# Performance work log

Measured on AMD Instinct MI355X. Metric: run time of the kernel, lower is better.

Reference implementation:

```python
import jax, jax.numpy as jnp
import numpy as np

D_MODEL = 1024
NUM_HEAD = 16
BATCH = 2
SEQ = 2048
NEG_INF = -1e9  # matches masked_fill value in the original


def setup_inputs() -> dict:
    key = jax.random.key(0)
    k1, k2, k3, k4, k5 = jax.random.split(key, 5)
    scale = 1.0 / np.sqrt(D_MODEL)
    return {
        "x": jax.random.normal(k1, (BATCH, SEQ, D_MODEL), dtype=jnp.float32),
        "q_weight": jax.random.normal(k2, (D_MODEL, D_MODEL), dtype=jnp.float32) * scale,
        "k_weight": jax.random.normal(k3, (D_MODEL, D_MODEL), dtype=jnp.float32) * scale,
        "v_weight": jax.random.normal(k4, (D_MODEL, D_MODEL), dtype=jnp.float32) * scale,
        "o_weight": jax.random.normal(k5, (D_MODEL, D_MODEL), dtype=jnp.float32) * scale,
    }


def reference(x, q_weight, k_weight, v_weight, o_weight):
    b, s, d = x.shape
    h = NUM_HEAD
    dh = d // h
    # projections: weight layout is (d_out, d_in)
    q = jnp.einsum('bsd,ed->bse', x, q_weight).reshape(b, s, h, dh).transpose(0, 2, 1, 3)
    k = jnp.einsum('bsd,ed->bse', x, k_weight).reshape(b, s, h, dh).transpose(0, 2, 1, 3)
    v = jnp.einsum('bsd,ed->bse', x, v_weight).reshape(b, s, h, dh).transpose(0, 2, 1, 3)
    scores = jnp.einsum('bhqd,bhkd->bhqk', q, k) / jnp.sqrt(jnp.asarray(dh, x.dtype))
    causal = jnp.triu(jnp.ones((s, s), dtype=bool), k=1)  # True above diagonal -> masked
    scores = jnp.where(causal, jnp.asarray(NEG_INF, x.dtype), scores)
    attn = jax.nn.softmax(scores, axis=-1)
    out = jnp.einsum('bhqk,bhkd->bhqd', attn, v)          # [b,h,s,dh]
    out = out.transpose(0, 2, 1, 3).reshape(b, s, d)       # merge heads
    return jnp.einsum('bse,de->bsd', out, o_weight)
```

## Files before the change

kernel.cpp:

```cpp
#include <hip/hip_runtime.h>

typedef short bhalf8 __attribute__((ext_vector_type(8)));
typedef float floatx4 __attribute__((ext_vector_type(4)));

#define D_MODEL 1024
#define SEQ     2048
#define BATCH   2
#define NHEAD   16
#define DH      64

#define GLDS(g, l) __builtin_amdgcn_global_load_lds( \
    (const __attribute__((address_space(1))) void*)(g), \
    (__attribute__((address_space(3))) void*)(l), 16, 0, 0)

static __device__ __forceinline__ short f2bf(float f) {
    unsigned u = __builtin_bit_cast(unsigned, f);
    u = (u + 0x7fffu + ((u >> 16) & 1u)) >> 16;
    return (short)u;
}
static __device__ __forceinline__ unsigned pack2(float a, float b) {
    return (unsigned)(unsigned short)f2bf(a) | ((unsigned)(unsigned short)f2bf(b) << 16);
}
static __device__ __forceinline__ unsigned cvt_pk_bf16(float lo, float hi) {
    unsigned r;
    asm("v_cvt_pk_bf16_f32 %0, %1, %2" : "=v"(r) : "v"(lo), "v"(hi));
    return r;
}

__global__ __launch_bounds__(256) void cast_all(const float* __restrict__ x,
                                                const float* __restrict__ wq,
                                                const float* __restrict__ wk,
                                                const float* __restrict__ wv,
                                                const float* __restrict__ wo,
                                                short* __restrict__ xb,
                                                short* __restrict__ wall) {
    const int bid = blockIdx.x;
    const float* s;
    short* d;
    int i;
    if (bid < 2048) {
        s = x; d = xb;
        i = (bid * 256 + threadIdx.x) * 8;
    } else {
        const int wb = bid - 2048;
        const int which = wb >> 9;
        s = (which == 0) ? wq : (which == 1) ? wk : (which == 2) ? wv : wo;
        d = wall + (size_t)which * (D_MODEL * D_MODEL);
        i = ((wb & 511) * 256 + threadIdx.x) * 8;
    }
    float4 a = *(const float4*)(s + i);
    float4 b = *(const float4*)(s + i + 4);
    uint4 u = {pack2(a.x, a.y), pack2(a.z, a.w), pack2(b.x, b.y), pack2(b.z, b.w)};
    *(uint4*)(d + i) = u;
}

#define MFMA_BF16 __builtin_amdgcn_mfma_f32_16x16x32_bf16

#define QISSUE(kt, s) do {                                                    \
    char* ab_ = pool + (s) * 16384 + (w * 32) * 64;                           \
    char* bb_ = pool + 49152 + (s) * 16384 + (w * 32) * 64;                   \
    GLDS(Ag + (size_t)(kt) * 32, ab_);                                        \
    GLDS(Ag + (size_t)(kt) * 32 + 16 * 1024, ab_ + 1024);                     \
    GLDS(Wg + (size_t)(kt) * 32, bb_);                                        \
    GLDS(Wg + (size_t)(kt) * 32 + 16 * 1024, bb_ + 1024);                     \
} while (0)

#define QCOMP(s) do {                                                         \
    const short(*As_)[32] = (const short(*)[32])(pool + (s) * 16384);         \
    const short(*Bs_)[32] = (const short(*)[32])(pool + 49152 + (s) * 16384); \
    bhalf8 af_[8], bf_[4];                                                    \
    _Pragma("unroll")                                                         \
    for (int m_ = 0; m_ < 8; ++m_)                                            \
        af_[m_] = *(const bhalf8*)&As_[wr * 128 + m_ * 16 + l16][quad * 8];   \
    _Pragma("unroll")                                                         \
    for (int n_ = 0; n_ < 4; ++n_)                                            \
        bf_[n_] = *(const bhalf8*)&Bs_[wc * 64 + n_ * 16 + l16][quad * 8];    \
    __builtin_amdgcn_s_setprio(1);                                            \
    _Pragma("unroll")                                                         \
    for (int m_ = 0; m_ < 8; ++m_)                                            \
        _Pragma("unroll")                                                     \
        for (int n_ = 0; n_ < 4; ++n_)                                        \
            acc[m_][n_] = MFMA_BF16(af_[m_], bf_[n_], acc[m_][n_], 0, 0, 0);  \
    __builtin_amdgcn_s_setprio(0);                                            \
} while (0)

__global__ __launch_bounds__(512) void gemm_qkv2(const short* __restrict__ A,
                                                 const short* __restrict__ W,
                                                 short* __restrict__ Qo,
                                                 short* __restrict__ Ko,
                                                 short* __restrict__ Vt) {
    __shared__ __align__(16) char pool[98304];
    const int t    = threadIdx.x;
    const int w    = t >> 6, lane = t & 63, quad = lane >> 4, l16 = lane & 15;
    const int wr   = w >> 2, wc = w & 3;
    const int bm   = blockIdx.x * 256;
    const int by   = (int)blockIdx.y;
    const int bn   = by * 256;

    const short* Ag = A + (size_t)(bm + w * 32 + (lane >> 2)) * 1024 + (lane & 3) * 8;
    const short* Wg = W + (size_t)(bn + w * 32 + (lane >> 2)) * 1024 + (lane & 3) * 8;

    floatx4 acc[8][4];
#pragma unroll
    for (int m = 0; m < 8; ++m)
#pragma unroll
        for (int n = 0; n < 4; ++n) {
            floatx4 z = {0.f, 0.f, 0.f, 0.f};
            acc[m][n] = z;
        }

    QISSUE(0, 0);
    QISSUE(1, 1);
    int sc_ = 0, sn_ = 2;
#pragma unroll 1
    for (int kt = 0; kt < 30; ++kt) {
        asm volatile("s_waitcnt vmcnt(4)" ::: "memory");
        __builtin_amdgcn_s_barrier();
        QISSUE(kt + 2, sn_);
        QCOMP(sc_);
        sc_ = (sc_ == 2) ? 0 : sc_ + 1;
        sn_ = (sn_ == 2) ? 0 : sn_ + 1;
    }
    asm volatile("s_waitcnt vmcnt(4)" ::: "memory");
    __builtin_amdgcn_s_barrier();
    QCOMP(sc_);
    sc_ = (sc_ == 2) ? 0 : sc_ + 1;
    asm volatile("s_waitcnt vmcnt(0)" ::: "memory");
    __builtin_amdgcn_s_barrier();
    QCOMP(sc_);

    __syncthreads();
    short (*Ct)[268] = (short(*)[268])pool;
    if (by < 8) {
        short* outp = (by < 4) ? Qo : Ko;
        const int colbase = (by < 4) ? bn : bn - 1024;
        for (int hh = 0; hh < 2; ++hh) {
            if (wr == hh) {
#pragma unroll
                for (int m = 0; m < 8; ++m)
#pragma unroll
                    for (int n = 0; n < 4; ++n)
#pragma unroll
                        for (int g = 0; g < 4; ++g)
                            Ct[m * 16 + quad * 4 + g][wc * 64 + n * 16 + l16] =
                                f2bf(acc[m][n][g]);
            }
            __syncthreads();
            {
                const int r = t >> 2, c0 = (t & 3) * 64;
#pragma unroll
                for (int p = 0; p < 8; ++p)
                    *(uint4*)(outp + (size_t)(bm + hh * 128 + r) * 1024 +
                              colbase + c0 + p * 8) =
                        *(const uint4*)&Ct[r][c0 + p * 8];
            }
            __syncthreads();
        }
    } else {
        const int nbase = bn - 2048;
        for (int hh = 0; hh < 2; ++hh) {
            if ((wc >> 1) == hh) {
#pragma unroll
                for (int m = 0; m < 8; ++m)
#pragma unroll
                    for (int n = 0; n < 4; ++n)
#pragma unroll
                        for (int g = 0; g < 4; ++g)
                            Ct[wc * 64 + n * 16 + l16 - hh * 128]
                              [wr * 128 + m * 16 + quad * 4 + g] =
                                f2bf(acc[m][n][g]);
            }
            __syncthreads();
            {
                const int r = t >> 2, c0 = (t & 3) * 64;
#pragma unroll
                for (int p = 0; p < 8; ++p)
                    *(uint4*)(Vt + (size_t)(nbase + hh * 128 + r) * 4096 +
                              bm + c0 + p * 8) =
                        *(const uint4*)&Ct[r][c0 + p * 8];
            }
            __syncthreads();
        }
    }
}

__global__ __launch_bounds__(256) void gemm_o(const short* __restrict__ A,
                                              const short* __restrict__ W,
                                              float* __restrict__ C) {
    __shared__ __align__(16) char pool[34816];
    short (*As)[64] = (short(*)[64])pool;
    short (*Bs)[64] = (short(*)[64])(pool + 16384);
    const int t    = threadIdx.x;
    const int wave = t >> 6, lane = t & 63, quad = lane >> 4, l16 = lane & 15;
    const int bm = blockIdx.x * 128, bn = blockIdx.y * 64;
    const int qm = (wave >> 1) * 64, qn = (wave & 1) * 32;

    const int lrow = lane >> 3, lcol = (lane & 7) * 8;
    const short* Ag = A + (size_t)(bm + wave * 32 + lrow) * 1024 + lcol;
    const short* Wg = W + (size_t)(bn + wave * 16 + lrow) * 1024 + lcol;
    short* Al = &As[wave * 32][0];
    short* Bl = &Bs[wave * 16][0];

    floatx4 acc[4][2];
#pragma unroll
    for (int i = 0; i < 4; ++i)
#pragma unroll
        for (int j = 0; j < 2; ++j) {
            floatx4 z = {0.f, 0.f, 0.f, 0.f};
            acc[i][j] = z;
        }

    for (int k0 = 0; k0 < 1024; k0 += 64) {
        __syncthreads();
#pragma unroll
        for (int j = 0; j < 4; ++j)
            GLDS(Ag + k0 + (size_t)j * 8 * 1024, Al + j * 8 * 64);
#pragma unroll
        for (int j = 0; j < 2; ++j)
            GLDS(Wg + k0 + (size_t)j * 8 * 1024, Bl + j * 8 * 64);
        __syncthreads();
#pragma unroll
        for (int kk = 0; kk < 64; kk += 32) {
            bhalf8 af[4], bfr[2];
#pragma unroll
            for (int im = 0; im < 4; ++im)
                af[im] = *(const bhalf8*)&As[qm + im * 16 + l16][kk + quad * 8];
#pragma unroll
            for (int jn = 0; jn < 2; ++jn)
                bfr[jn] = *(const bhalf8*)&Bs[qn + jn * 16 + l16][kk + quad * 8];
#pragma unroll
            for (int im = 0; im < 4; ++im)
#pragma unroll
                for (int jn = 0; jn < 2; ++jn)
                    acc[im][jn] = __builtin_amdgcn_mfma_f32_16x16x32_bf16(
                        af[im], bfr[jn], acc[im][jn], 0, 0, 0);
        }
    }

    __syncthreads();
    float (*Ctf)[68] = (float(*)[68])pool;
#pragma unroll
    for (int im = 0; im < 4; ++im)
#pragma unroll
        for (int jn = 0; jn < 2; ++jn)
#pragma unroll
            for (int g = 0; g < 4; ++g)
                Ctf[qm + im * 16 + quad * 4 + g][qn + jn * 16 + l16] = acc[im][jn][g];
    __syncthreads();
#pragma unroll
    for (int pass = 0; pass < 8; ++pass) {
        const int r = (t >> 4) + pass * 16;
        const int c = (t & 15) * 4;
        float4 u = *(const float4*)&Ctf[r][c];
        *(float4*)(C + (size_t)(bm + r) * 1024 + bn + c) = u;
    }
}


#define STAGE_LOAD(kregv, vregv, kk) do {                                     \
    kregv = *(const uint4*)(Kbase + (size_t)((kk) + sr) * 1024 + sc);         \
    vregv = *(const uint4*)(Vbase + (size_t)sr * 4096 + (kk) + sc);           \
    } while (0)

#define STAGE_WRITE(bufv, kregv, vregv) do {                                  \
    *(uint4*)&Ks[bufv][sr][sc] = kregv;                                       \
    *(uint4*)&Vs[bufv][sr][sc] = vregv;                                       \
    } while (0)

#define CHUNK13(bufv, k0v, qwv) do {                                          \
    bhalf8 kf_[4][2];                                                         \
    _Pragma("unroll")                                                         \
    for (int jn_ = 0; jn_ < 4; ++jn_) {                                       \
        kf_[jn_][0] = *(const bhalf8*)&Ks[bufv][jn_ * 16 + l16][quad * 8];    \
        kf_[jn_][1] = *(const bhalf8*)&Ks[bufv][jn_ * 16 + l16][32 + quad * 8]; \
    }                                                                         \
    floatx4 s_[4];                                                            \
    _Pragma("unroll")                                                         \
    for (int jn_ = 0; jn_ < 4; ++jn_) {                                       \
        floatx4 z_ = {0.f, 0.f, 0.f, 0.f};                                    \
        z_ = MFMA_BF16(qf0, kf_[jn_][0], z_, 0, 0, 0);                        \
        z_ = MFMA_BF16(qf1, kf_[jn_][1], z_, 0, 0, 0);                        \
        s_[jn_] = z_;                                                         \
    }                                                                         \
    bhalf8 vf_[4][2];              \
    _Pragma("unroll")                                                         \
    for (int nd_ = 0; nd_ < 4; ++nd_) {                                       \
        vf_[nd_][0] = *(const bhalf8*)&Vs[bufv][nd_ * 16 + l16][quad * 8];    \
        vf_[nd_][1] = *(const bhalf8*)&Vs[bufv][nd_ * 16 + l16][32 + quad * 8]; \
    }                                                                         \
    const bool partial_ = ((k0v) + 64 > (qwv));                               \
    _Pragma("unroll")                                                         \
    for (int g_ = 0; g_ < 4; ++g_) {                                          \
        const int rr_ = quad * 4 + g_;                                        \
        const int qrow_ = (qwv) + rr_;                                        \
        float e0_ = exp2f(s_[0][g_] * KS - CB);                               \
        float e1_ = exp2f(s_[1][g_] * KS - CB);                               \
        float e2_ = exp2f(s_[2][g_] * KS - CB);                               \
        float e3_ = exp2f(s_[3][g_] * KS - CB);                               \
        if (partial_) {                                                       \
            if ((k0v) + l16 > qrow_)      e0_ = 0.f;                          \
            if ((k0v) + 16 + l16 > qrow_) e1_ = 0.f;                          \
            if ((k0v) + 32 + l16 > qrow_) e2_ = 0.f;                          \
            if ((k0v) + 48 + l16 > qrow_) e3_ = 0.f;                          \
        }                                                                     \
        lsum[g_] += (e0_ + e1_) + (e2_ + e3_);                                \
        unsigned r01_ = cvt_pk_bf16(e0_, e1_);                                \
        unsigned r23_ = cvt_pk_bf16(e2_, e3_);                                \
        Ps[wave][rr_][l16]      = (short)r01_;                                \
        Ps[wave][rr_][16 + l16] = (short)(r01_ >> 16);                        \
        Ps[wave][rr_][32 + l16] = (short)r23_;                                \
        Ps[wave][rr_][48 + l16] = (short)(r23_ >> 16);                        \
    }                                                                         \
          \
    bhalf8 ap0_ = *(const bhalf8*)&Ps[wave][l16][quad * 8];                   \
    bhalf8 ap1_ = *(const bhalf8*)&Ps[wave][l16][32 + quad * 8];              \
    _Pragma("unroll")                                                         \
    for (int nd_ = 0; nd_ < 4; ++nd_) {                                       \
        o[nd_] = MFMA_BF16(ap0_, vf_[nd_][0], o[nd_], 0, 0, 0);               \
        o[nd_] = MFMA_BF16(ap1_, vf_[nd_][1], o[nd_], 0, 0, 0);               \
    }                                                                         \
} while (0)

#define SWEEP(qtv, ncv) do {                                                  \
    const int qw_ = (qtv) * 128 + wave * 16;                                  \
    const short* qr_ = Qbase + (size_t)(qw_ + l16) * 1024;                    \
    bhalf8 qf0 = *(const bhalf8*)(qr_ + quad * 8);                            \
    bhalf8 qf1 = *(const bhalf8*)(qr_ + 32 + quad * 8);                       \
    _Pragma("unroll")                                                         \
    for (int g_ = 0; g_ < 4; ++g_) lsum[g_] = 0.f;                            \
    _Pragma("unroll")                                                         \
    for (int nd_ = 0; nd_ < 4; ++nd_) {                                       \
        floatx4 z_ = {0.f, 0.f, 0.f, 0.f};                                    \
        o[nd_] = z_;                                                          \
    }                                                                         \
    uint4 kreg_, vreg_;                                                       \
    STAGE_LOAD(kreg_, vreg_, 0);                                              \
    STAGE_WRITE(0, kreg_, vreg_);                                             \
    if ((ncv) > 1) STAGE_LOAD(kreg_, vreg_, 64);                              \
    __syncthreads();                                                          \
    _Pragma("unroll 1")                                                       \
    for (int i_ = 0; i_ < (ncv); ++i_) {                                      \
        const int buf_ = i_ & 1;                                              \
        if (i_ + 1 < (ncv)) STAGE_WRITE(buf_ ^ 1, kreg_, vreg_);              \
        if (i_ + 2 < (ncv)) STAGE_LOAD(kreg_, vreg_, (i_ + 2) * 64);          \
        CHUNK13(buf_, i_ * 64, qw_);                                          \
        __syncthreads();                                                      \
    }                                                                         \
    _Pragma("unroll")                                                         \
    for (int g_ = 0; g_ < 4; ++g_) {                                          \
        float r_ = lsum[g_];                                                  \
        r_ += __shfl_xor(r_, 1, 64);                                          \
        r_ += __shfl_xor(r_, 2, 64);                                          \
        r_ += __shfl_xor(r_, 4, 64);                                          \
        r_ += __shfl_xor(r_, 8, 64);                                          \
        const float iv_ = 1.0f / r_;                                          \
        const int qrow_ = qw_ + quad * 4 + g_;                                \
        _Pragma("unroll")                                                     \
        for (int nd_ = 0; nd_ < 4; ++nd_)                                     \
            Y[(size_t)(b * SEQ + qrow_) * 1024 + h * 64 + nd_ * 16 + l16] =   \
                f2bf(o[nd_][g_] * iv_);                                       \
    }                                                                         \
} while (0)

__global__ __launch_bounds__(512) void attn_v14(const short* __restrict__ Qo,
                                                const short* __restrict__ Ko,
                                                const short* __restrict__ Vt,
                                                short* __restrict__ Y) {
    __shared__ __align__(16) short Ks[2][64][72];
    __shared__ __align__(16) short Vs[2][64][72];
    __shared__ __align__(16) short Ps[8][16][72];

    const int t    = threadIdx.x;
    const int wave = t >> 6, lane = t & 63, quad = lane >> 4, l16 = lane & 15;
    const int bid  = (int)blockIdx.x;
    const int bh   = bid & 31;
    const int p    = (bid & 255) >> 5;
    const int qt   = (bid < 256) ? (15 - p) : p;
    const int b = bh >> 4, h = bh & 15;

    const short* Qbase = Qo + (size_t)b * SEQ * 1024 + h * 64;
    const short* Kbase = Ko + (size_t)b * SEQ * 1024 + h * 64;
    const short* Vbase = Vt + (size_t)h * 64 * 4096 + (size_t)b * SEQ;

    const int sr = t >> 3;
    const int sc = (t & 7) * 8;

    const float KS = 0.125f * 1.44269504f;
    const float CB = 12.0f * 1.44269504f;

    float lsum[4];
    floatx4 o[4];

    SWEEP(qt, (qt + 1) * 2);
}

extern "C" void kernel_launch(void* const* d_in, const int* in_sizes, int n_in,
                              void* d_out, int out_size, void* d_ws, size_t ws_size,
                              hipStream_t stream) {
    const float* x  = (const float*)d_in[0];
    const float* wq = (const float*)d_in[1];
    const float* wk = (const float*)d_in[2];
    const float* wv = (const float*)d_in[3];
    const float* wo = (const float*)d_in[4];

    short* xb   = (short*)d_ws;
    short* Qo   = xb + (size_t)4096 * 1024;
    short* Ko   = Qo + (size_t)4096 * 1024;
    short* Vt   = Ko + (size_t)4096 * 1024;
    short* wall = Vt + (size_t)1024 * 4096;
    short* wob  = wall + (size_t)3 * 1024 * 1024;

    cast_all<<<dim3(4096), 256, 0, stream>>>(x, wq, wk, wv, wo, xb, wall);
    gemm_qkv2<<<dim3(16, 12), 512, 0, stream>>>(xb, wall, Qo, Ko, Vt);
    attn_v14<<<dim3(512), 512, 0, stream>>>(Qo, Ko, Vt, xb);
    gemm_o<<<dim3(32, 16), 256, 0, stream>>>(xb, wob, (float*)d_out);
}
```

Measured before the change: 190.1 us.

## Split attention key range across two wave teams with per-wave 32-row Q tiles

Restructures the attention kernel so each block's 8 waves form two teams of 4. Each team processes half of the causal key range in 32-key chunks. Each wave now owns 32 query rows instead of 16, so K fragments are reused across two row tiles. The teams' partial O and row-sum results are combined through shared memory before normalisation. The aim is to shorten the serial key loop per block and raise MFMA reuse, at the cost of an extra LDS combine step, more registers, and wasted work when a team's chunks are fully masked. The block-to-query-tile ordering is also reversed.

```diff
diff --git a/kernel.cpp b/kernel.cpp
--- a/kernel.cpp
+++ b/kernel.cpp
@@ -257,141 +257,174 @@
 }
 
 
-#define STAGE_LOAD(kregv, vregv, kk) do {                                     \
-    kregv = *(const uint4*)(Kbase + (size_t)((kk) + sr) * 1024 + sc);         \
-    vregv = *(const uint4*)(Vbase + (size_t)sr * 4096 + (kk) + sc);           \
+#define STAGE_LOAD15(kk) do {                                                 \
+    kreg = *(const uint4*)(Kbase + (size_t)((kk) + skr) * 1024 + skc);        \
+    vreg = *(const uint4*)(Vbase + (size_t)svr * 4096 + (kk) + svc);          \
     } while (0)
 
-#define STAGE_WRITE(bufv, kregv, vregv) do {                                  \
-    *(uint4*)&Ks[bufv][sr][sc] = kregv;                                       \
-    *(uint4*)&Vs[bufv][sr][sc] = vregv;                                       \
+#define STAGE_WRITE15(bufv) do {                                              \
+    *(uint4*)&Ks[team][bufv][skr][skc] = kreg;                                \
+    *(uint4*)&Vs[team][bufv][svr][svc] = vreg;                                \
     } while (0)
 
-#define CHUNK13(bufv, k0v, qwv) do {                                          \
-    bhalf8 kf_[4][2];                                                         \
-    _Pragma("unroll")                                                         \
-    for (int jn_ = 0; jn_ < 4; ++jn_) {                                       \
-        kf_[jn_][0] = *(const bhalf8*)&Ks[bufv][jn_ * 16 + l16][quad * 8];    \
-        kf_[jn_][1] = *(const bhalf8*)&Ks[bufv][jn_ * 16 + l16][32 + quad * 8]; \
+#define CHUNK15(bufv, k0v) do {                                               \
+    bhalf8 kf_[2][2];                                                         \
+    _Pragma("unroll")                                                         \
+    for (int jn_ = 0; jn_ < 2; ++jn_) {                                       \
+        kf_[jn_][0] = *(const bhalf8*)&Ks[team][bufv][jn_ * 16 + l16][quad * 8]; \
+        kf_[jn_][1] = *(const bhalf8*)&Ks[team][bufv][jn_ * 16 + l16][32 + quad * 8]; \
     }                                                                         \
-    floatx4 s_[4];                                                            \
-    _Pragma("unroll")                                                         \
-    for (int jn_ = 0; jn_ < 4; ++jn_) {                                       \
-        floatx4 z_ = {0.f, 0.f, 0.f, 0.f};                                    \
-        z_ = MFMA_BF16(qf0, kf_[jn_][0], z_, 0, 0, 0);                        \
-        z_ = MFMA_BF16(qf1, kf_[jn_][1], z_, 0, 0, 0);                        \
-        s_[jn_] = z_;                                                         \
-    }                                                                         \
-    bhalf8 vf_[4][2];              \
-    _Pragma("unroll")                                                         \
-    for (int nd_ = 0; nd_ < 4; ++nd_) {                                       \
-        vf_[nd_][0] = *(const bhalf8*)&Vs[bufv][nd_ * 16 + l16][quad * 8];    \
-        vf_[nd_][1] = *(const bhalf8*)&Vs[bufv][nd_ * 16 + l16][32 + quad * 8]; \
-    }                                                                         \
-    const bool partial_ = ((k0v) + 64 > (qwv));                               \
-    _Pragma("unroll")                                                         \
-    for (int g_ = 0; g_ < 4; ++g_) {                                          \
-        const int rr_ = quad * 4 + g_;                                        \
-        const int qrow_ = (qwv) + rr_;                                        \
-        float e0_ = exp2f(s_[0][g_] * KS - CB);                               \
-        float e1_ = exp2f(s_[1][g_] * KS - CB);                               \
-        float e2_ = exp2f(s_[2][g_] * KS - CB);                               \
-        float e3_ = exp2f(s_[3][g_] * KS - CB);                               \
-        if (partial_) {                                                       \
-            if ((k0v) + l16 > qrow_)      e0_ = 0.f;                          \
-            if ((k0v) + 16 + l16 > qrow_) e1_ = 0.f;                          \
-            if ((k0v) + 32 + l16 > qrow_) e2_ = 0.f;                          \
-            if ((k0v) + 48 + l16 > qrow_) e3_ = 0.f;                          \
+    floatx4 s_[2][2];                                                         \
+    _Pragma("unroll")                                                         \
+    for (int im_ = 0; im_ < 2; ++im_)                                         \
+        _Pragma("unroll")                                                     \
+        for (int jn_ = 0; jn_ < 2; ++jn_) {                                   \
+            floatx4 z_ = {0.f, 0.f, 0.f, 0.f};                                \
+            z_ = MFMA_BF16(qf[im_][0], kf_[jn_][0], z_, 0, 0, 0);             \
+            z_ = MFMA_BF16(qf[im_][1], kf_[jn_][1], z_, 0, 0, 0);             \
+            s_[im_][jn_] = z_;                                                \
         }                                                                     \
-        lsum[g_] += (e0_ + e1_) + (e2_ + e3_);                                \
-        unsigned r01_ = cvt_pk_bf16(e0_, e1_);                                \
-        unsigned r23_ = cvt_pk_bf16(e2_, e3_);                                \
-        Ps[wave][rr_][l16]      = (short)r01_;                                \
-        Ps[wave][rr_][16 + l16] = (short)(r01_ >> 16);                        \
-        Ps[wave][rr_][32 + l16] = (short)r23_;                                \
-        Ps[wave][rr_][48 + l16] = (short)(r23_ >> 16);                        \
-    }                                                                         \
+    const bool partial_ = ((k0v) + 32 > qw_);                                 \
+    _Pragma("unroll")                                                         \
+    for (int im_ = 0; im_ < 2; ++im_)                                         \
+        _Pragma("unroll")                                                     \
+        for (int g_ = 0; g_ < 4; ++g_) {                                      \
+            const int rr_ = im_ * 16 + quad * 4 + g_;                         \
+            const int qrow_ = qw_ + rr_;                                      \
+            float e0_ = exp2f(s_[im_][0][g_] * KS - CB);                      \
+            float e1_ = exp2f(s_[im_][1][g_] * KS - CB);                      \
+            if (partial_) {                                                   \
+                if ((k0v) + l16 > qrow_)      e0_ = 0.f;                      \
+                if ((k0v) + 16 + l16 > qrow_) e1_ = 0.f;                      \
+            }                                                                 \
+            lsum[im_][g_] += e0_ + e1_;                                       \
+            unsigned r01_ = cvt_pk_bf16(e0_, e1_);                            \
+            Ps[wave][rr_][l16]      = (short)r01_;                            \
+            Ps[wave][rr_][16 + l16] = (short)(r01_ >> 16);                    \
+        }                                                                     \
           \
-    bhalf8 ap0_ = *(const bhalf8*)&Ps[wave][l16][quad * 8];                   \
-    bhalf8 ap1_ = *(const bhalf8*)&Ps[wave][l16][32 + quad * 8];              \
-    _Pragma("unroll")                                                         \
-    for (int nd_ = 0; nd_ < 4; ++nd_) {                                       \
-        o[nd_] = MFMA_BF16(ap0_, vf_[nd_][0], o[nd_], 0, 0, 0);               \
-        o[nd_] = MFMA_BF16(ap1_, vf_[nd_][1], o[nd_], 0, 0, 0);               \
-    }                                                                         \
-} while (0)
-
-#define SWEEP(qtv, ncv) do {                                                  \
-    const int qw_ = (qtv) * 128 + wave * 16;                                  \
-    const short* qr_ = Qbase + (size_t)(qw_ + l16) * 1024;                    \
-    bhalf8 qf0 = *(const bhalf8*)(qr_ + quad * 8);                            \
-    bhalf8 qf1 = *(const bhalf8*)(qr_ + 32 + quad * 8);                       \
-    _Pragma("unroll")                                                         \
-    for (int g_ = 0; g_ < 4; ++g_) lsum[g_] = 0.f;                            \
-    _Pragma("unroll")                                                         \
-    for (int nd_ = 0; nd_ < 4; ++nd_) {                                       \
-        floatx4 z_ = {0.f, 0.f, 0.f, 0.f};                                    \
-        o[nd_] = z_;                                                          \
-    }                                                                         \
-    uint4 kreg_, vreg_;                                                       \
-    STAGE_LOAD(kreg_, vreg_, 0);                                              \
-    STAGE_WRITE(0, kreg_, vreg_);                                             \
-    if ((ncv) > 1) STAGE_LOAD(kreg_, vreg_, 64);                              \
-    __syncthreads();                                                          \
-    _Pragma("unroll 1")                                                       \
-    for (int i_ = 0; i_ < (ncv); ++i_) {                                      \
-        const int buf_ = i_ & 1;                                              \
-        if (i_ + 1 < (ncv)) STAGE_WRITE(buf_ ^ 1, kreg_, vreg_);              \
-        if (i_ + 2 < (ncv)) STAGE_LOAD(kreg_, vreg_, (i_ + 2) * 64);          \
-        CHUNK13(buf_, i_ * 64, qw_);                                          \
-        __syncthreads();                                                      \
-    }                                                                         \
-    _Pragma("unroll")                                                         \
-    for (int g_ = 0; g_ < 4; ++g_) {                                          \
-        float r_ = lsum[g_];                                                  \
-        r_ += __shfl_xor(r_, 1, 64);                                          \
-        r_ += __shfl_xor(r_, 2, 64);                                          \
-        r_ += __shfl_xor(r_, 4, 64);                                          \
-        r_ += __shfl_xor(r_, 8, 64);                                          \
-        const float iv_ = 1.0f / r_;                                          \
-        const int qrow_ = qw_ + quad * 4 + g_;                                \
+    bhalf8 vf_[4];                                                            \
+    _Pragma("unroll")                                                         \
+    for (int nd_ = 0; nd_ < 4; ++nd_)                                         \
+        vf_[nd_] = *(const bhalf8*)&Vs[team][bufv][nd_ * 16 + l16][quad * 8]; \
+    bhalf8 ap_[2];                                                            \
+    _Pragma("unroll")                                                         \
+    for (int im_ = 0; im_ < 2; ++im_)                                         \
+        ap_[im_] = *(const bhalf8*)&Ps[wave][im_ * 16 + l16][quad * 8];       \
+    _Pragma("unroll")                                                         \
+    for (int im_ = 0; im_ < 2; ++im_)                                         \
         _Pragma("unroll")                                                     \
         for (int nd_ = 0; nd_ < 4; ++nd_)                                     \
-            Y[(size_t)(b * SEQ + qrow_) * 1024 + h * 64 + nd_ * 16 + l16] =   \
-                f2bf(o[nd_][g_] * iv_);                                       \
-    }                                                                         \
+            o[im_][nd_] = MFMA_BF16(ap_[im_], vf_[nd_], o[im_][nd_], 0, 0, 0); \
 } while (0)
 
-__global__ __launch_bounds__(512) void attn_v14(const short* __restrict__ Qo,
+__global__ __launch_bounds__(512) void attn_v15(const short* __restrict__ Qo,
                                                 const short* __restrict__ Ko,
                                                 const short* __restrict__ Vt,
                                                 short* __restrict__ Y) {
-    __shared__ __align__(16) short Ks[2][64][72];
-    __shared__ __align__(16) short Vs[2][64][72];
-    __shared__ __align__(16) short Ps[8][16][72];
+    __shared__ __align__(16) char pool[59392];
+    short (*Ks)[2][32][72] = (short(*)[2][32][72])pool;
+    short (*Vs)[2][64][40] = (short(*)[2][64][40])(pool + 18432);
+    short (*Ps)[32][40]    = (short(*)[32][40])(pool + 38912);
+    float (*Cmb)[64][44]   = (float(*)[64][44])pool;
 
     const int t    = threadIdx.x;
     const int wave = t >> 6, lane = t & 63, quad = lane >> 4, l16 = lane & 15;
+    const int team = t >> 8, wt = wave & 3, tt = t & 255;
     const int bid  = (int)blockIdx.x;
     const int bh   = bid & 31;
-    const int p    = (bid & 255) >> 5;
-    const int qt   = (bid < 256) ? (15 - p) : p;
+    const int qt   = (bid < 256) ? (bid >> 5) : (15 - ((bid - 256) >> 5));
     const int b = bh >> 4, h = bh & 15;
+    const int nct   = (qt + 1) * 2;
+    const int kbase = team * nct * 32;
 
     const short* Qbase = Qo + (size_t)b * SEQ * 1024 + h * 64;
     const short* Kbase = Ko + (size_t)b * SEQ * 1024 + h * 64;
     const short* Vbase = Vt + (size_t)h * 64 * 4096 + (size_t)b * SEQ;
 
-    const int sr = t >> 3;
-    const int sc = (t & 7) * 8;
+    const int skr = tt >> 3, skc = (tt & 7) * 8;
+    const int svr = tt >> 2, svc = (tt & 3) * 8;
 
     const float KS = 0.125f * 1.44269504f;
     const float CB = 12.0f * 1.44269504f;
 
-    float lsum[4];
-    floatx4 o[4];
-
-    SWEEP(qt, (qt + 1) * 2);
+    const int qw_ = qt * 128 + wt * 32;
+    bhalf8 qf[2][2];
+#pragma unroll
+    for (int im = 0; im < 2; ++im) {
+        const short* qr = Qbase + (size_t)(qw_ + im * 16 + l16) * 1024;
+        qf[im][0] = *(const bhalf8*)(qr + quad * 8);
+        qf[im][1] = *(const bhalf8*)(qr + 32 + quad * 8);
+    }
+
+    float lsum[2][4];
+    floatx4 o[2][4];
+#pragma unroll
+    for (int im = 0; im < 2; ++im) {
+#pragma unroll
+        for (int g = 0; g < 4; ++g) lsum[im][g] = 0.f;
+#pragma unroll
+        for (int nd = 0; nd < 4; ++nd) {
+            floatx4 z = {0.f, 0.f, 0.f, 0.f};
+            o[im][nd] = z;
+        }
+    }
+
+    uint4 kreg, vreg;
+    STAGE_LOAD15(kbase);
+    STAGE_WRITE15(0);
+    if (nct > 1) STAGE_LOAD15(kbase + 32);
+    __syncthreads();
+#pragma unroll 1
+    for (int i = 0; i < nct; ++i) {
+        const int buf = i & 1;
+        if (i + 1 < nct) STAGE_WRITE15(buf ^ 1);
+        if (i + 2 < nct) STAGE_LOAD15(kbase + (i + 2) * 32);
+        const int k0 = kbase + i * 32;
+        if (k0 <= qw_ + 31) {
+            CHUNK15(buf, k0);
+        }
+        __syncthreads();
+    }
+
+    if (team == 1) {
+        float* cp = &Cmb[wt][lane][0];
+#pragma unroll
+        for (int im = 0; im < 2; ++im)
+#pragma unroll
+            for (int nd = 0; nd < 4; ++nd)
+                *(floatx4*)(cp + (im * 4 + nd) * 4) = o[im][nd];
+#pragma unroll
+        for (int im = 0; im < 2; ++im)
+#pragma unroll
+            for (int g = 0; g < 4; ++g)
+                cp[32 + im * 4 + g] = lsum[im][g];
+    }
+    __syncthreads();
+    if (team == 0) {
+        const float* cp = &Cmb[wt][lane][0];
+#pragma unroll
+        for (int im = 0; im < 2; ++im)
+#pragma unroll
+            for (int nd = 0; nd < 4; ++nd)
+                o[im][nd] += *(const floatx4*)(cp + (im * 4 + nd) * 4);
+#pragma unroll
+        for (int im = 0; im < 2; ++im)
+#pragma unroll
+            for (int g = 0; g < 4; ++g) {
+                float r = lsum[im][g] + cp[32 + im * 4 + g];
+                r += __shfl_xor(r, 1, 64);
+                r += __shfl_xor(r, 2, 64);
+                r += __shfl_xor(r, 4, 64);
+                r += __shfl_xor(r, 8, 64);
+                const float iv = 1.0f / r;
+                const int qrow = qw_ + im * 16 + quad * 4 + g;
+#pragma unroll
+                for (int nd = 0; nd < 4; ++nd)
+                    Y[(size_t)(b * SEQ + qrow) * 1024 + h * 64 + nd * 16 + l16] =
+                        f2bf(o[im][nd][g] * iv);
+            }
+    }
 }
 
 extern "C" void kernel_launch(void* const* d_in, const int* in_sizes, int n_in,
@@ -412,6 +445,6 @@
 
     cast_all<<<dim3(4096), 256, 0, stream>>>(x, wq, wk, wv, wo, xb, wall);
     gemm_qkv2<<<dim3(16, 12), 512, 0, stream>>>(xb, wall, Qo, Ko, Vt);
-    attn_v14<<<dim3(512), 512, 0, stream>>>(Qo, Ko, Vt, xb);
+    attn_v15<<<dim3(512), 512, 0, stream>>>(Qo, Ko, Vt, xb);
     gemm_o<<<dim3(32, 16), 256, 0, stream>>>(xb, wob, (float*)d_out);
 }
```

Measured after the change: 191.4 us. About the same (+0.7%).
